# Kernel optimization log

Hardware: AMD Instinct MI355X
Metric: run time of the kernel (lower is better)

The kernel has to match this reference:

```python
import jax, jax.numpy as jnp
import numpy as np
from jax import lax

# dims: B batch, V views, D feature dim, C classes, P prompts
B, V, D, C, P = 512, 10, 1024, 100, 4
ADAPTER_RATIO = 0.6
EPS = 0.01          # sinkhorn entropic regularizer (compute_logits default)
MAX_ITER = 1000     # compute_logits default
THRESH = 1e-2       # PLOT Sinkhorn early-stop threshold on |r - r_prev|.mean()
BN_EPS = 1e-5


def setup_inputs() -> dict:
    key = jax.random.key(0)
    ks = jax.random.split(key, 8)
    # Correlated features so cosine similarity ~0.9 (realistic CLIP-like sims);
    # keeps exp(-wdist/0.01) well inside fp32 range for the Sinkhorn solver.
    base = jax.random.normal(ks[0], (D,), jnp.float32)
    feat = base[None, :] + 0.3 * jax.random.normal(ks[1], (B * V, D), jnp.float32)
    text_feat = base[None, None, :] + 0.3 * jax.random.normal(ks[2], (C, P, D), jnp.float32)
    w = lambda k, shp: 0.02 * jax.random.normal(k, shp, jnp.float32)
    return {
        "feat": feat,                       # (B*V, D) CLIP visual features
        "text_feat": text_feat,             # (C, P, D) encoded text features
        "fusion_ratio": jnp.full((V,), 0.5, jnp.float32),
        "bn1_gamma": jnp.ones((D,), jnp.float32),
        "bn1_beta": jnp.zeros((D,), jnp.float32),
        "W_glob": w(ks[3], (D, D * V)),     # Linear(D*V -> D), torch layout (out, in)
        "b_glob": jnp.zeros((D,), jnp.float32),
        "bn2_gamma": jnp.ones((D,), jnp.float32),
        "bn2_beta": jnp.zeros((D,), jnp.float32),
        "W_v1": w(ks[4], (D, D)),           # Linear(D -> D)
        "b_v1": jnp.zeros((D,), jnp.float32),
        "W_v2": w(ks[5], (D * V, D)),       # Linear(D -> D*V)
        "b_v2": jnp.zeros((D * V,), jnp.float32),
        "logit_scale": jnp.array(np.log(1.0 / 0.07), jnp.float32),
    }


def _bn_train(x, gamma, beta):
    # BatchNorm1d in training mode: biased batch statistics over axis 0
    m = x.mean(axis=0)
    v = x.var(axis=0)
    return (x - m) * lax.rsqrt(v + BN_EPS) * gamma + beta


def _adapter(feat, fusion_ratio, bn1_g, bn1_b, Wg, bg, bn2_g, bn2_b, Wv1, bv1, Wv2, bv2):
    img = feat.reshape(-1, V, D)
    res = feat.reshape(-1, V * D)
    x = img * fusion_ratio.reshape(1, -1, 1)          # per-view fusion weights
    x = _bn_train(x.reshape(-1, D), bn1_g, bn1_b)     # BatchNormPoint over D
    x = x.reshape(-1, V * D)                          # Flatten
    g = jax.nn.relu(_bn_train(x @ Wg.T + bg, bn2_g, bn2_b))   # global_f (dropout=0)
    view = jax.nn.relu(jax.nn.relu(g @ Wv1.T + bv1) @ Wv2.T + bv2)  # view_f
    return view * ADAPTER_RATIO + res * (1.0 - ADAPTER_RATIO)


def _sinkhorn(K, p, q):
    # PLOT-style Sinkhorn: r = p / (K c); c = q / (K^T r); early stop on mean |dr|
    r0 = jnp.ones_like(p)
    c0 = jnp.ones_like(q)

    def cond(st):
        i, r, c, err = st
        return jnp.logical_and(i < MAX_ITER, err > THRESH)

    def body(st):
        i, r, c, _ = st
        r_prev = r
        r = p / jnp.einsum('nvp,np->nv', K, c)
        c = q / jnp.einsum('nvp,nv->np', K, r)
        err = jnp.mean(jnp.abs(r - r_prev))
        return i + 1, r, c, err

    _, r, c, _ = lax.while_loop(cond, body, (jnp.int32(0), r0, c0, jnp.float32(jnp.inf)))
    return r[:, :, None] * K * c[:, None, :]   # T = diag(r) K diag(c)


def reference(feat, text_feat, fusion_ratio, bn1_gamma, bn1_beta, W_glob, b_glob,
              bn2_gamma, bn2_beta, W_v1, b_v1, W_v2, b_v2, logit_scale):
    img_feat = _adapter(feat, fusion_ratio, bn1_gamma, bn1_beta, W_glob, b_glob,
                        bn2_gamma, bn2_beta, W_v1, b_v1, W_v2, b_v2)
    img_feat = img_feat.reshape(-1, V, D)
    img_feat = img_feat / jnp.linalg.norm(img_feat, axis=-1, keepdims=True)
    txt = text_feat / jnp.linalg.norm(text_feat, axis=-1, keepdims=True)

    # compute_logits: sim (B, C, V, P) -> (B*C, V, P)
    sim = jnp.einsum('bvd,cpd->bcvp', img_feat, txt).reshape(B * C, V, P)
    wdist = 1.0 - sim
    p = jnp.full((B * C, V), 1.0 / V, sim.dtype)
    q = jnp.full((B * C, P), 1.0 / P, sim.dtype)
    K = jnp.exp(-wdist / EPS)
    T = _sinkhorn(lax.stop_gradient(K), p, q)   # solver runs under no_grad
    d_OT = jnp.sum(T * wdist, axis=(1, 2)).reshape(B, C)
    logits = jnp.exp(logit_scale) * (1.0 - d_OT)
    return logits
```

## Files before the change

kernel.cpp:

```cpp
#include <hip/hip_runtime.h>
#include <cstdint>


typedef unsigned short u16;
typedef __attribute__((ext_vector_type(8))) short bf8v;
typedef __attribute__((ext_vector_type(4))) float f4v;

__device__ __forceinline__ float4 ld4(const float* p){ return *reinterpret_cast<const float4*>(p); }
__device__ __forceinline__ void st4(float* p, float4 v){ *reinterpret_cast<float4*>(p) = v; }
__device__ __forceinline__ u16 f2bf(float x){
  uint32_t u = __float_as_uint(x);
  return (u16)((u + 0x7FFFu + ((u>>16)&1u)) >> 16);
}
__device__ __forceinline__ uint32_t pk(float a, float b){
  return (uint32_t)f2bf(a) | ((uint32_t)f2bf(b)<<16);
}
__device__ __forceinline__ void glds16(const u16* g, u16* l){
  __builtin_amdgcn_global_load_lds(
      (const __attribute__((address_space(1))) unsigned int*)g,
      (__attribute__((address_space(3))) unsigned int*)l, 16, 0, 0);
}

__global__ __launch_bounds__(256,4)
void gemm_bf16_nt(const u16* __restrict__ A, const u16* __restrict__ B,
                  float* __restrict__ C, int lda, int ldb, int ldc,
                  int kLen, long strideCz, int map, int NBX, int NBY)
{
  __shared__ u16 As0[2048], Bs0[4096], As1[2048], Bs1[4096];
  const int tid = threadIdx.x, lane = tid & 63, w = tid >> 6;

  int bx, by, bz;
  if (map == 0){ bx = blockIdx.x; by = blockIdx.y; bz = blockIdx.z; }
  else {
    const int i = blockIdx.x, xcd = i & 7, j = i >> 3;
    if (map == 1){
      const int mnC = NBX*NBY;
      const int zPer = (gridDim.x >> 3) / mnC;
      bz = xcd*zPer + j/mnC;
      const int mn = j % mnC; bx = mn % NBX; by = mn / NBX;
    } else {
      const int nbxPer = NBX >> 3;
      bx = xcd*nbxPer + j % nbxPer; by = j / nbxPer; bz = 0;
    }
  }

  const long bm = (long)by*64, bn = (long)bx*128;
  const long kz = (long)bz*kLen;
  C += (long)bz*strideCz;

  const int srow  = lane>>2;
  const int sslot = (lane&3) ^ ((lane>>3)&3);
  const u16* Ag = A + (bm + w*16 + srow)*(long)lda + kz + sslot*8;
  const u16* Bg = B + (bn + w*32 + srow)*(long)ldb + kz + sslot*8;
  const long b16 = 16L*ldb;
  const int woffA = w*512, woffB = w*1024;

  const int fr = lane & 15;
  const int rslot = ((lane>>4) ^ ((lane>>1)&3))*16;
  const int wr = (w>>1)*32, wc = (w&1)*64;

  const f4v zero = {0.f,0.f,0.f,0.f};
  f4v acc[2][4];
  #pragma unroll
  for (int i2=0;i2<2;i2++)
    #pragma unroll
    for (int j2=0;j2<4;j2++) acc[i2][j2]=zero;

  auto STAGE = [&](u16* Al, u16* Bl, int kt){
    glds16(Ag + kt,       Al + woffA);
    glds16(Bg + kt,       Bl + woffB);
    glds16(Bg + kt + b16, Bl + woffB + 512);
  };
  auto COMPUTE = [&](const u16* Asb, const u16* Bsb){
    bf8v af[2], bf[4];
    #pragma unroll
    for (int mi=0; mi<2; ++mi)
      af[mi] = *(const bf8v*)((const char*)Asb + (wr+mi*16+fr)*64 + rslot);
    #pragma unroll
    for (int nj=0; nj<4; ++nj)
      bf[nj] = *(const bf8v*)((const char*)Bsb + (wc+nj*16+fr)*64 + rslot);
    #pragma unroll
    for (int mi=0; mi<2; ++mi)
      #pragma unroll
      for (int nj=0; nj<4; ++nj)
        acc[mi][nj] = __builtin_amdgcn_mfma_f32_16x16x32_bf16(af[mi], bf[nj], acc[mi][nj], 0,0,0);
  };

  STAGE(As0, Bs0, 0);
  __syncthreads();
  int kt = 32;
  for (; kt < kLen - 32; kt += 64){
    STAGE(As1, Bs1, kt);
    COMPUTE(As0, Bs0);
    __syncthreads();
    STAGE(As0, Bs0, kt + 32);
    COMPUTE(As1, Bs1);
    __syncthreads();
  }
  STAGE(As1, Bs1, kt);
  COMPUTE(As0, Bs0);
  __syncthreads();
  COMPUTE(As1, Bs1);

  const int orow = (lane>>4)*4;
  #pragma unroll
  for (int mi=0;mi<2;++mi){
    #pragma unroll
    for (int q=0;q<4;++q){
      const long row = bm + wr + mi*16 + orow + q;
      float* Crow = C + row*(long)ldc + bn + wc + fr;
      #pragma unroll
      for (int nj=0;nj<4;++nj) Crow[nj*16] = acc[mi][nj][q];
    }
  }
}

__global__ __launch_bounds__(256)
void cvt_bf16(const float* __restrict__ in, u16* __restrict__ out, long n8)
{
  for (long i = (long)blockIdx.x*256 + threadIdx.x; i < n8; i += (long)gridDim.x*256){
    const float4 a = ld4(&in[i*8]), b = ld4(&in[i*8+4]);
    uint4 o;
    o.x = pk(a.x,a.y); o.y = pk(a.z,a.w);
    o.z = pk(b.x,b.y); o.w = pk(b.z,b.w);
    *reinterpret_cast<uint4*>(&out[i*8]) = o;
  }
}

__global__ __launch_bounds__(256)
void reduce_f32(const float* __restrict__ P, int S, int MN,
                const float* __restrict__ bias, float* __restrict__ out)
{
  const long i = ((long)blockIdx.x*256 + threadIdx.x)*4;
  float4 s = ld4(&P[i]);
  for (int z=1; z<S; ++z){
    const float4 v = ld4(&P[(long)z*MN + i]);
    s.x+=v.x; s.y+=v.y; s.z+=v.z; s.w+=v.w;
  }
  const float4 b = ld4(&bias[(int)(i & 1023)]);
  s.x+=b.x; s.y+=b.y; s.z+=b.z; s.w+=b.w;
  st4(&out[i], s);
}

__global__ __launch_bounds__(256)
void reduce_bf16(const float* __restrict__ P, int S, int MN,
                 const float* __restrict__ bias, u16* __restrict__ out)
{
  const long i = ((long)blockIdx.x*256 + threadIdx.x)*4;
  float4 s = ld4(&P[i]);
  for (int z=1; z<S; ++z){
    const float4 v = ld4(&P[(long)z*MN + i]);
    s.x+=v.x; s.y+=v.y; s.z+=v.z; s.w+=v.w;
  }
  const float4 b = ld4(&bias[(int)(i & 1023)]);
  s.x = fmaxf(s.x+b.x,0.f); s.y = fmaxf(s.y+b.y,0.f);
  s.z = fmaxf(s.z+b.z,0.f); s.w = fmaxf(s.w+b.w,0.f);
  uint2 o; o.x = pk(s.x,s.y); o.y = pk(s.z,s.w);
  *reinterpret_cast<uint2*>(&out[i]) = o;
}

__global__ __launch_bounds__(256)
void colstats_p1(const float* __restrict__ X, int rpb, const float* __restrict__ fr,
                 float* __restrict__ part)
{
  const int c = threadIdx.x*4;
  const long r0 = (long)blockIdx.x*rpb;
  float4 s = make_float4(0,0,0,0), q = make_float4(0,0,0,0);
  for (int rr=0; rr<rpb; ++rr){
    const long r = r0+rr;
    float4 x = ld4(&X[r*1024 + c]);
    if (fr){ const float f = fr[(int)(r%10)]; x.x*=f; x.y*=f; x.z*=f; x.w*=f; }
    s.x+=x.x; s.y+=x.y; s.z+=x.z; s.w+=x.w;
    q.x+=x.x*x.x; q.y+=x.y*x.y; q.z+=x.z*x.z; q.w+=x.w*x.w;
  }
  float* p = part + (long)blockIdx.x*2048;
  st4(&p[c], s);
  st4(&p[1024+c], q);
}

__global__ __launch_bounds__(256)
void colstats_reduce(const float* __restrict__ in, float* __restrict__ out,
                     int nslab, int chunk)
{
  const int idx = blockIdx.x*256 + threadIdx.x;
  const int s0 = blockIdx.y*chunk;
  const int s1 = min(nslab, s0+chunk);
  float a0=0.f, a1=0.f, a2=0.f, a3=0.f;
  int s = s0;
  for (; s+4 <= s1; s += 4){
    a0 += in[(long)s*2048+idx];
    a1 += in[(long)(s+1)*2048+idx];
    a2 += in[(long)(s+2)*2048+idx];
    a3 += in[(long)(s+3)*2048+idx];
  }
  for (; s < s1; ++s) a0 += in[(long)s*2048+idx];
  out[(long)blockIdx.y*2048 + idx] = (a0+a1)+(a2+a3);
}

__global__ __launch_bounds__(256)
void bn_apply_bf16(const float* __restrict__ X, const float* __restrict__ fr,
                   const float* __restrict__ stats, float invN,
                   const float* __restrict__ gamma,
                   const float* __restrict__ beta, int relu, u16* __restrict__ out)
{
  const long i = ((long)blockIdx.x*256 + threadIdx.x)*4;
  const int d = (int)(i & 1023);
  const float4 s  = ld4(&stats[d]);
  const float4 qq = ld4(&stats[1024+d]);
  const float4 gm = ld4(&gamma[d]);
  const float4 bt = ld4(&beta[d]);
  float4 sc, sh;
  { const float m=s.x*invN, v=qq.x*invN-m*m; sc.x=gm.x*rsqrtf(v+1e-5f); sh.x=bt.x-m*sc.x; }
  { const float m=s.y*invN, v=qq.y*invN-m*m; sc.y=gm.y*rsqrtf(v+1e-5f); sh.y=bt.y-m*sc.y; }
  { const float m=s.z*invN, v=qq.z*invN-m*m; sc.z=gm.z*rsqrtf(v+1e-5f); sh.z=bt.z-m*sc.z; }
  { const float m=s.w*invN, v=qq.w*invN-m*m; sc.w=gm.w*rsqrtf(v+1e-5f); sh.w=bt.w-m*sc.w; }
  float4 x = ld4(&X[i]);
  if (fr){ const float f = fr[(int)((i>>10)%10)]; x.x*=f; x.y*=f; x.z*=f; x.w*=f; }
  x.x = x.x*sc.x + sh.x; x.y = x.y*sc.y + sh.y;
  x.z = x.z*sc.z + sh.z; x.w = x.w*sc.w + sh.w;
  if (relu){ x.x=fmaxf(x.x,0.f); x.y=fmaxf(x.y,0.f); x.z=fmaxf(x.z,0.f); x.w=fmaxf(x.w,0.f); }
  uint2 o; o.x = pk(x.x,x.y); o.y = pk(x.z,x.w);
  *reinterpret_cast<uint2*>(&out[i]) = o;
}

__device__ __forceinline__ float blockSum256(float v, float* sh4){
  #pragma unroll
  for (int m=32; m; m>>=1) v += __shfl_xor(v, m, 64);
  const int w = threadIdx.x >> 6;
  if ((threadIdx.x & 63) == 0) sh4[w] = v;
  __syncthreads();
  return sh4[0]+sh4[1]+sh4[2]+sh4[3];
}

__global__ __launch_bounds__(256)
void rownorm_bf16(const float* __restrict__ X, u16* __restrict__ out)
{
  __shared__ float sh4[4];
  const int row = blockIdx.x;
  const int d = threadIdx.x*4;
  if (row >= 400){ *reinterpret_cast<uint2*>(&out[(long)row*1024 + d]) = make_uint2(0,0); return; }
  const long base = (long)row*1024 + d;
  const float4 x = ld4(&X[base]);
  const float ss = x.x*x.x + x.y*x.y + x.z*x.z + x.w*x.w;
  const float rn = rsqrtf(blockSum256(ss, sh4));
  uint2 o; o.x = pk(x.x*rn, x.y*rn); o.y = pk(x.z*rn, x.w*rn);
  *reinterpret_cast<uint2*>(&out[base]) = o;
}

__global__ __launch_bounds__(256)
void mix_norm_bf16(const float* __restrict__ P, const float* __restrict__ feat,
                   const float* __restrict__ bv2, u16* __restrict__ outp)
{
  __shared__ float sh4[4];
  const int m = blockIdx.x;
  const int v = m % 10;
  const long base = (long)m*1024;
  const int d = threadIdx.x*4;
  const float4 y  = ld4(&P[base+d]);
  const float4 bb = ld4(&bv2[v*1024 + d]);
  const float4 f  = ld4(&feat[base+d]);
  float4 img;
  img.x = 0.6f*fmaxf(y.x+bb.x,0.f) + 0.4f*f.x;
  img.y = 0.6f*fmaxf(y.y+bb.y,0.f) + 0.4f*f.y;
  img.z = 0.6f*fmaxf(y.z+bb.z,0.f) + 0.4f*f.z;
  img.w = 0.6f*fmaxf(y.w+bb.w,0.f) + 0.4f*f.w;
  const float ss = img.x*img.x + img.y*img.y + img.z*img.z + img.w*img.w;
  const float rn = rsqrtf(blockSum256(ss, sh4));
  uint2 o; o.x = pk(img.x*rn, img.y*rn); o.y = pk(img.z*rn, img.w*rn);
  *reinterpret_cast<uint2*>(&outp[base+d]) = o;
}

__global__ __launch_bounds__(256)
void sinkhorn_solve(const float* __restrict__ sim, const float* __restrict__ lsp,
                    float* __restrict__ out)
{
  const int n = blockIdx.x*256 + threadIdx.x;
  const int b = n / 100, c = n % 100;
  float S[10][4], Km[10][4];
  #pragma unroll
  for (int v=0; v<10; ++v){
    const long off = (long)(b*10+v)*512 + c*4;
    const float4 a0 = ld4(&sim[off]);
    const float4 a1 = ld4(&sim[2621440L + off]);
    S[v][0]=a0.x+a1.x; S[v][1]=a0.y+a1.y; S[v][2]=a0.z+a1.z; S[v][3]=a0.w+a1.w;
    #pragma unroll
    for (int p=0;p<4;++p) Km[v][p] = expf((S[v][p]-1.f)*100.f);
  }
  float r[10], cc[4];
  #pragma unroll
  for (int v=0;v<10;++v) r[v]=1.f;
  #pragma unroll
  for (int p=0;p<4;++p) cc[p]=1.f;
  for (int j=0; j<1000; ++j){
    float lerr = 0.f;
    #pragma unroll
    for (int v=0;v<10;++v){
      const float s = Km[v][0]*cc[0]+Km[v][1]*cc[1]+Km[v][2]*cc[2]+Km[v][3]*cc[3];
      const float rn = __fdividef(0.1f, s);
      lerr += fabsf(rn - r[v]); r[v]=rn;
    }
    #pragma unroll
    for (int p=0;p<4;++p){
      float s = 0.f;
      #pragma unroll
      for (int v=0;v<10;++v) s += Km[v][p]*r[v];
      cc[p] = __fdividef(0.25f, s);
    }
    float w = lerr;
    #pragma unroll
    for (int m=32; m; m>>=1) w += __shfl_xor(w, m, 64);
    if (w <= 0.25f) break;
  }
  float dOT = 0.f;
  #pragma unroll
  for (int v=0;v<10;++v)
    #pragma unroll
    for (int p=0;p<4;++p)
      dOT += r[v]*Km[v][p]*cc[p]*(1.f - S[v][p]);
  out[n] = expf(lsp[0]) * (1.f - dOT);
}

extern "C" void kernel_launch(void* const* d_in, const int* in_sizes, int n_in,
                              void* d_out, int out_size, void* d_ws, size_t ws_size,
                              hipStream_t stream)
{
  const float* feat  = (const float*)d_in[0];
  const float* textf = (const float*)d_in[1];
  const float* fr    = (const float*)d_in[2];
  const float* bn1g  = (const float*)d_in[3];
  const float* bn1b  = (const float*)d_in[4];
  const float* Wg    = (const float*)d_in[5];
  const float* bg    = (const float*)d_in[6];
  const float* bn2g  = (const float*)d_in[7];
  const float* bn2b  = (const float*)d_in[8];
  const float* Wv1   = (const float*)d_in[9];
  const float* bv1   = (const float*)d_in[10];
  const float* Wv2   = (const float*)d_in[11];
  const float* bv2   = (const float*)d_in[12];
  const float* ls    = (const float*)d_in[13];
  float* out = (float*)d_out;
  char* base = (char*)d_ws;

  u16*   WB  = (u16*)(base + 0);
  u16*   Xb  = (u16*)(base + 20971520);
  float* P   = (float*)(base + 31457280);
  float* P2  = P + 1310720;
  u16*   W1b = (u16*)(base + 65011712);
  float* y1  = (float*)(base + 67108864);
  u16*   Gb  = (u16*)(base + 69206016);
  u16*   Hb  = (u16*)(base + 70254592);
  u16*   Tb  = (u16*)(base + 71303168);
  float* ex  = (float*)(base + 72351744);
  float* bn1st=ex, *bn2st=ex+2048;

  cvt_bf16<<<2048,256,0,stream>>>(Wg, WB, 1310720);

  colstats_p1<<<640,256,0,stream>>>(feat, 8, fr, P);
  colstats_reduce<<<dim3(8,20),256,0,stream>>>(P, P2, 640, 32);
  colstats_reduce<<<dim3(8,1),256,0,stream>>>(P2, bn1st, 20, 20);
  bn_apply_bf16<<<5120,256,0,stream>>>(feat, fr, bn1st, 1.f/5120.f,
                                       bn1g, bn1b, 0, Xb);

  gemm_bf16_nt<<<1024,256,0,stream>>>(Xb, WB, P, 10240,10240,1024, 640, 524288L,
                                      1, 8, 8);
  reduce_f32<<<512,256,0,stream>>>(P, 16, 524288, bg, y1);

  colstats_p1<<<128,256,0,stream>>>(y1, 4, nullptr, P);
  colstats_reduce<<<dim3(8,8),256,0,stream>>>(P, P2, 128, 16);
  colstats_reduce<<<dim3(8,1),256,0,stream>>>(P2, bn2st, 8, 8);
  bn_apply_bf16<<<512,256,0,stream>>>(y1, nullptr, bn2st, 1.f/512.f,
                                      bn2g, bn2b, 1, Gb);
  cvt_bf16<<<512,256,0,stream>>>(Wv1, W1b, 131072);

  gemm_bf16_nt<<<512,256,0,stream>>>(Gb, W1b, P, 1024,1024,1024, 128, 524288L,
                                     1, 8, 8);
  reduce_bf16<<<512,256,0,stream>>>(P, 8, 524288, bv1, Hb);

  cvt_bf16<<<2048,256,0,stream>>>(Wv2, WB, 1310720);

  gemm_bf16_nt<<<640,256,0,stream>>>(Hb, WB, P, 1024,1024,10240, 1024, 0L,
                                     2, 80, 8);
  mix_norm_bf16<<<5120,256,0,stream>>>(P, feat, bv2, Xb);

  rownorm_bf16<<<512,256,0,stream>>>(textf, Tb);
  gemm_bf16_nt<<<dim3(4,80,2),256,0,stream>>>(Xb, Tb, P, 1024,1024,512, 512,
                                              2621440L, 0, 0, 0);

  sinkhorn_solve<<<200,256,0,stream>>>(P, ls, out);
}
```

Measured before the change: 152.8 us.

## Fuse weight conversions, fold BN2 stats into split-K reduce, retune Sinkhorn

Merges the Wg and Wv1 fp32-to-bf16 conversions into one launch. Folds the per-row sum and sum-of-squares for the second batchnorm into the split-K reduction kernel, which removes a separate colstats pass over y1 at the cost of writing a larger partial buffer. Shrinks the Sinkhorn blocks to 64 threads so more blocks spread across CUs. It also checks the convergence reduction only every other iteration, which saves shuffles but can run one extra iteration per wave.

```diff
diff --git a/kernel.cpp b/kernel.cpp
--- a/kernel.cpp
+++ b/kernel.cpp
@@ -21,6 +21,22 @@
       (__attribute__((address_space(3))) unsigned int*)l, 16, 0, 0);
 }
 
+__device__ __forceinline__ void remap(int map, int NBX, int NBY,
+                                      int& bx, int& by, int& bz)
+{
+  if (map == 0){ bx = blockIdx.x; by = blockIdx.y; bz = blockIdx.z; return; }
+  const int i = blockIdx.x, xcd = i & 7, j = i >> 3;
+  if (map == 1){
+    const int mnC = NBX*NBY;
+    const int zPer = (gridDim.x >> 3) / mnC;
+    bz = xcd*zPer + j/mnC;
+    const int mn = j % mnC; bx = mn % NBX; by = mn / NBX;
+  } else {
+    const int nbxPer = NBX >> 3;
+    bx = xcd*nbxPer + j % nbxPer; by = j / nbxPer; bz = 0;
+  }
+}
+
 __global__ __launch_bounds__(256,4)
 void gemm_bf16_nt(const u16* __restrict__ A, const u16* __restrict__ B,
                   float* __restrict__ C, int lda, int ldb, int ldc,
@@ -28,21 +44,7 @@
 {
   __shared__ u16 As0[2048], Bs0[4096], As1[2048], Bs1[4096];
   const int tid = threadIdx.x, lane = tid & 63, w = tid >> 6;
-
-  int bx, by, bz;
-  if (map == 0){ bx = blockIdx.x; by = blockIdx.y; bz = blockIdx.z; }
-  else {
-    const int i = blockIdx.x, xcd = i & 7, j = i >> 3;
-    if (map == 1){
-      const int mnC = NBX*NBY;
-      const int zPer = (gridDim.x >> 3) / mnC;
-      bz = xcd*zPer + j/mnC;
-      const int mn = j % mnC; bx = mn % NBX; by = mn / NBX;
-    } else {
-      const int nbxPer = NBX >> 3;
-      bx = xcd*nbxPer + j % nbxPer; by = j / nbxPer; bz = 0;
-    }
-  }
+  int bx, by, bz; remap(map, NBX, NBY, bx, by, bz);
 
   const long bm = (long)by*64, bn = (long)bx*128;
   const long kz = (long)bz*kLen;
@@ -116,6 +118,24 @@
 }
 
 __global__ __launch_bounds__(256)
+void cvt_w(const float* __restrict__ Wg, const float* __restrict__ Wv1,
+           u16* __restrict__ WB, u16* __restrict__ W1b)
+{
+  const long NG = 1310720;
+  const long NT = NG + 131072;
+  for (long i = (long)blockIdx.x*256 + threadIdx.x; i < NT; i += (long)gridDim.x*256){
+    const float* src; u16* dst; long k;
+    if (i < NG){ src = Wg; dst = WB; k = i; }
+    else       { src = Wv1; dst = W1b; k = i - NG; }
+    const float4 a = ld4(&src[k*8]), b = ld4(&src[k*8+4]);
+    uint4 o;
+    o.x = pk(a.x,a.y); o.y = pk(a.z,a.w);
+    o.z = pk(b.x,b.y); o.w = pk(b.z,b.w);
+    *reinterpret_cast<uint4*>(&dst[k*8]) = o;
+  }
+}
+
+__global__ __launch_bounds__(256)
 void cvt_bf16(const float* __restrict__ in, u16* __restrict__ out, long n8)
 {
   for (long i = (long)blockIdx.x*256 + threadIdx.x; i < n8; i += (long)gridDim.x*256){
@@ -128,18 +148,23 @@
 }
 
 __global__ __launch_bounds__(256)
-void reduce_f32(const float* __restrict__ P, int S, int MN,
-                const float* __restrict__ bias, float* __restrict__ out)
-{
-  const long i = ((long)blockIdx.x*256 + threadIdx.x)*4;
+void reduce_f32_stats(const float* __restrict__ P, int S, int MN,
+                      const float* __restrict__ bias, float* __restrict__ out,
+                      float* __restrict__ part)
+{
+  const int b = blockIdx.x, t = threadIdx.x;
+  const long i = (long)b*1024 + t*4;
   float4 s = ld4(&P[i]);
   for (int z=1; z<S; ++z){
     const float4 v = ld4(&P[(long)z*MN + i]);
     s.x+=v.x; s.y+=v.y; s.z+=v.z; s.w+=v.w;
   }
-  const float4 b = ld4(&bias[(int)(i & 1023)]);
-  s.x+=b.x; s.y+=b.y; s.z+=b.z; s.w+=b.w;
+  const float4 bb = ld4(&bias[t*4]);
+  s.x+=bb.x; s.y+=bb.y; s.z+=bb.z; s.w+=bb.w;
   st4(&out[i], s);
+  float* p = part + (long)b*2048;
+  st4(&p[t*4], s);
+  st4(&p[1024+t*4], make_float4(s.x*s.x, s.y*s.y, s.z*s.z, s.w*s.w));
 }
 
 __global__ __launch_bounds__(256)
@@ -270,11 +295,11 @@
   *reinterpret_cast<uint2*>(&outp[base+d]) = o;
 }
 
-__global__ __launch_bounds__(256)
+__global__ __launch_bounds__(64)
 void sinkhorn_solve(const float* __restrict__ sim, const float* __restrict__ lsp,
                     float* __restrict__ out)
 {
-  const int n = blockIdx.x*256 + threadIdx.x;
+  const int n = blockIdx.x*64 + threadIdx.x;
   const int b = n / 100, c = n % 100;
   float S[10][4], Km[10][4];
   #pragma unroll
@@ -306,10 +331,12 @@
       for (int v=0;v<10;++v) s += Km[v][p]*r[v];
       cc[p] = __fdividef(0.25f, s);
     }
-    float w = lerr;
-    #pragma unroll
-    for (int m=32; m; m>>=1) w += __shfl_xor(w, m, 64);
-    if (w <= 0.25f) break;
+    if (j & 1){
+      float w = lerr;
+      #pragma unroll
+      for (int m=32; m; m>>=1) w += __shfl_xor(w, m, 64);
+      if (w <= 0.25f) break;
+    }
   }
   float dOT = 0.f;
   #pragma unroll
@@ -352,8 +379,10 @@
   u16*   Tb  = (u16*)(base + 71303168);
   float* ex  = (float*)(base + 72351744);
   float* bn1st=ex, *bn2st=ex+2048;
-
-  cvt_bf16<<<2048,256,0,stream>>>(Wg, WB, 1310720);
+  float* partY = ex + 4096;
+  float* partY2= partY + 1048576;
+
+  cvt_w<<<2048,256,0,stream>>>(Wg, Wv1, WB, W1b);
 
   colstats_p1<<<640,256,0,stream>>>(feat, 8, fr, P);
   colstats_reduce<<<dim3(8,20),256,0,stream>>>(P, P2, 640, 32);
@@ -361,19 +390,16 @@
   bn_apply_bf16<<<5120,256,0,stream>>>(feat, fr, bn1st, 1.f/5120.f,
                                        bn1g, bn1b, 0, Xb);
 
-  gemm_bf16_nt<<<1024,256,0,stream>>>(Xb, WB, P, 10240,10240,1024, 640, 524288L,
-                                      1, 8, 8);
-  reduce_f32<<<512,256,0,stream>>>(P, 16, 524288, bg, y1);
-
-  colstats_p1<<<128,256,0,stream>>>(y1, 4, nullptr, P);
-  colstats_reduce<<<dim3(8,8),256,0,stream>>>(P, P2, 128, 16);
-  colstats_reduce<<<dim3(8,1),256,0,stream>>>(P2, bn2st, 8, 8);
+  gemm_bf16_nt<<<1024,256,0,stream>>>(Xb, WB, P, 10240,10240,1024, 640,
+                                      524288L, 1, 8, 8);
+  reduce_f32_stats<<<512,256,0,stream>>>(P, 16, 524288, bg, y1, partY);
+  colstats_reduce<<<dim3(8,16),256,0,stream>>>(partY, partY2, 512, 32);
+  colstats_reduce<<<dim3(8,1),256,0,stream>>>(partY2, bn2st, 16, 16);
   bn_apply_bf16<<<512,256,0,stream>>>(y1, nullptr, bn2st, 1.f/512.f,
                                       bn2g, bn2b, 1, Gb);
-  cvt_bf16<<<512,256,0,stream>>>(Wv1, W1b, 131072);
-
-  gemm_bf16_nt<<<512,256,0,stream>>>(Gb, W1b, P, 1024,1024,1024, 128, 524288L,
-                                     1, 8, 8);
+
+  gemm_bf16_nt<<<512,256,0,stream>>>(Gb, W1b, P, 1024,1024,1024, 128,
+                                     524288L, 1, 8, 8);
   reduce_bf16<<<512,256,0,stream>>>(P, 8, 524288, bv1, Hb);
 
   cvt_bf16<<<2048,256,0,stream>>>(Wv2, WB, 1310720);
@@ -386,5 +412,5 @@
   gemm_bf16_nt<<<dim3(4,80,2),256,0,stream>>>(Xb, Tb, P, 1024,1024,512, 512,
                                               2621440L, 0, 0, 0);
 
-  sinkhorn_solve<<<200,256,0,stream>>>(P, ls, out);
-}
+  sinkhorn_solve<<<800,64,0,stream>>>(P, ls, out);
+}
```

After: 154.1 us. No clear change (+0.8%).
